# Optimization experiments

Hardware: AMD Instinct MI355X
Metric: run time of the kernel (lower is better)

The kernel has to match this reference:

```python
import jax, jax.numpy as jnp
import numpy as np
from jax import lax

MAX_SIGMA = 20.0
TRUNCATE = 4.0  # scipy.ndimage.gaussian_filter default
R = int(TRUNCATE * MAX_SIGMA + 0.5)  # fixed max radius = 80 -> 161 taps


def setup_inputs() -> dict:
    key = jax.random.key(0)
    k1, k2 = jax.random.split(key)
    x = jax.random.normal(k1, (512, 256, 256), dtype=jnp.float32)
    blur_sigmas = jnp.geomspace(0.5, MAX_SIGMA, 32).astype(jnp.float32)
    fwd_steps = jax.random.randint(k2, (512,), 0, 32)
    return {"x": x, "blur_sigmas": blur_sigmas, "fwd_steps": fwd_steps}


def _per_sample_kernels(sigmas):
    # scipy gaussian_filter: radius_i = int(truncate*sigma + 0.5), kernel
    # phi(o) = exp(-o^2 / (2 sigma^2)) normalized over |o| <= radius_i.
    off = jnp.arange(-R, R + 1, dtype=jnp.float32)          # [2R+1]
    w = jnp.exp(-0.5 * (off[None, :] / sigmas[:, None]) ** 2)  # [B, 2R+1]
    rad = jnp.floor(TRUNCATE * sigmas + 0.5)[:, None]        # per-sample radius
    w = w * (jnp.abs(off)[None, :] <= rad)
    return w / jnp.sum(w, axis=-1, keepdims=True)


def _blur(x, kernels):
    # x: [B, H, W]; kernels: [B, 2R+1]. Separable depthwise conv, batch as
    # channels with feature_group_count=B; symmetric pad == scipy 'reflect'.
    B = x.shape[0]
    dn = ("NCHW", "OIHW", "NCHW")
    xp = jnp.pad(x, ((0, 0), (R, R), (R, R)), mode="symmetric")[None]  # [1,B,H+2R,W+2R]
    kh = kernels[:, None, :, None]  # [B,1,2R+1,1]
    kw = kernels[:, None, None, :]  # [B,1,1,2R+1]
    y = lax.conv_general_dilated(xp, kh, (1, 1), "VALID",
                                 dimension_numbers=dn, feature_group_count=B)
    y = lax.conv_general_dilated(y, kw, (1, 1), "VALID",
                                 dimension_numbers=dn, feature_group_count=B)
    return y[0]  # [B, H, W]


def reference(x, blur_sigmas, fwd_steps):
    sigmas = blur_sigmas[fwd_steps]           # [B] per-sample sigma
    kernels = _per_sample_kernels(sigmas)     # [B, 2R+1]
    return _blur(x, kernels)
```

## Files before the change

kernel.cpp:

```cpp
#include <hip/hip_runtime.h>

#define WDIM  256
#define NSAMP 512
#define NSIG  32
#define RB    64
#define NBAND 2048
#define QOFF  16
#define WOFF  65536

typedef float    f32x4 __attribute__((ext_vector_type(4)));
typedef _Float16 f16x8 __attribute__((ext_vector_type(8)));

__device__ __forceinline__ int reflect(int q) {
    q = (q < 0) ? (-q - 1) : q;
    return (q >= WDIM) ? (2 * WDIM - 1 - q) : q;
}

__global__ __launch_bounds__(256) void build_w(const float* __restrict__ sigmas,
                                               _Float16* __restrict__ Wg) {
    __shared__ float wl[161];
    __shared__ float red;
    int s = blockIdx.x, t = threadIdx.x;
    float sigma = sigmas[s];
    float radf = floorf(4.0f * sigma + 0.5f);
    if (t < 161) {
        float off = (float)(t - 80);
        float w = 0.0f;
        if (fabsf(off) <= radf) { float z = off / sigma; w = expf(-0.5f * z * z); }
        wl[t] = w;
    }
    __syncthreads();
    if (t < 64) {
        float v = wl[t] + wl[t + 64] + (t < 33 ? wl[t + 128] : 0.0f);
        #pragma unroll
        for (int o = 32; o > 0; o >>= 1) v += __shfl_down(v, o);
        if (t == 0) red = 1.0f / v;
    }
    __syncthreads();
    float rs = red;
    int i = t;
    _Float16* wrow = Wg + ((size_t)s << 16) + (i << 8);
    for (int rq = blockIdx.y * 4; rq < blockIdx.y * 4 + 4; ++rq) {
        f16x8 v;
        #pragma unroll
        for (int j = 0; j < 8; ++j) {
            int r = rq * 8 + j;
            int d1 = r - i, d2 = -r - 1 - i, d3 = 511 - r - i;
            float w = 0.0f;
            if (d1 >= -80 && d1 <= 80) w += wl[d1 + 80];
            if (d2 >= -80)             w += wl[d2 + 80];
            if (d3 <= 80)              w += wl[d3 + 80];
            v[j] = (_Float16)(w * rs);
        }
        *(f16x8*)(wrow + rq * 8) = v;
    }
}

__global__ void build_queue(const float* __restrict__ sigmas,
                            const int* __restrict__ steps,
                            int* __restrict__ q) {
    __shared__ int hist[32];
    __shared__ int base[32];
    int t = threadIdx.x;
    if (t < 32) hist[t] = 0;
    __syncthreads();
    int nb2[2], rd2[2], st2[2];
    #pragma unroll
    for (int k = 0; k < 2; ++k) {
        int samp = t + 256 * k;
        int st = steps[samp];
        float sigma = sigmas[st];
        int rad = (int)floorf(4.0f * sigma + 0.5f);
        st2[k] = st; rd2[k] = rad;
        nb2[k] = (2 * rad + 15) >> 3;
        atomicAdd(&hist[nb2[k]], 1);
    }
    __syncthreads();
    if (t == 0) {
        int acc = 0;
        for (int bin = 31; bin >= 0; --bin) { base[bin] = acc; acc += hist[bin]; }
    }
    __syncthreads();
    #pragma unroll
    for (int k = 0; k < 2; ++k) {
        int samp = t + 256 * k;
        int r = atomicAdd(&base[nb2[k]], 1);
        int x = r & 7;
        int p = r >> 3;
        #pragma unroll
        for (int jb = 0; jb < 4; ++jb)
            q[QOFF + (((p << 2) + jb) << 3) + x] =
                samp | (jb << 9) | (st2[k] << 11) | (rd2[k] << 16);
    }
}

template <bool QUEUED>
__global__ __launch_bounds__(256, 2) void blur_mfma(const float* __restrict__ in,
                                                    float* __restrict__ out,
                                                    const float* __restrict__ sigmas,
                                                    const int* __restrict__ steps,
                                                    const int* __restrict__ q,
                                                    const _Float16* __restrict__ Wg) {
    __shared__ alignas(16) _Float16 YL[RB * WDIM];

    int b, r0, s, rad;
    if constexpr (QUEUED) {
        int d = q[QOFF + blockIdx.x];
        b   = d & 511;
        r0  = ((d >> 9) & 3) << 6;
        s   = (d >> 11) & 31;
        rad = (d >> 16) & 127;
    } else {
        int bid = blockIdx.x;
        int e = (bid & 7) * (NBAND / 8) + (bid >> 3);
        b = e >> 2; r0 = (e & 3) * RB;
        s = steps[b];
        rad = (int)floorf(4.0f * sigmas[s] + 0.5f);
    }
    const _Float16* Wm = Wg + ((size_t)s << 16);
    const float*    Xb = in + ((size_t)b << 16);

    int ln = threadIdx.x & 63, wv = threadIdx.x >> 6;
    int lm = ln & 15, lq = ln >> 4;

    f32x4 acc[4][4];
    #pragma unroll
    for (int mt = 0; mt < 4; ++mt)
        #pragma unroll
        for (int nt = 0; nt < 4; ++nt) acc[mt][nt] = (f32x4)0.0f;

    int kt0 = max(0, r0 - rad) >> 5;
    int kt1 = min(WDIM - 1, r0 + RB - 1 + rad) >> 5;

    float xvc[4][8], xvn[4][8];

    auto xload = [&](int kt, float (&dst)[4][8]) {
        const float* xp = Xb + (size_t)((kt << 5) + lq * 8) * WDIM + wv * 64 + lm;
        #pragma unroll
        for (int nt = 0; nt < 4; ++nt)
            #pragma unroll
            for (int jj = 0; jj < 8; ++jj)
                dst[nt][jj] = xp[(size_t)jj * WDIM + nt * 16];
    };
    auto vtile = [&](int kt, float (&xv)[4][8]) {
        f16x8 af[4];
        #pragma unroll
        for (int mt = 0; mt < 4; ++mt)
            af[mt] = *(const f16x8*)(Wm + (size_t)(r0 + mt * 16 + lm) * WDIM + (kt << 5) + lq * 8);
        #pragma unroll
        for (int nt = 0; nt < 4; ++nt) {
            f16x8 bf;
            #pragma unroll
            for (int jj = 0; jj < 8; ++jj) bf[jj] = (_Float16)xv[nt][jj];
            #pragma unroll
            for (int mt = 0; mt < 4; ++mt)
                acc[mt][nt] = __builtin_amdgcn_mfma_f32_16x16x32_f16(af[mt], bf, acc[mt][nt], 0, 0, 0);
        }
    };

    xload(kt0, xvc);
    for (int kt = kt0; kt <= kt1; ++kt) {
        if (kt < kt1) xload(kt + 1, xvn);
        vtile(kt, xvc);
        if (kt < kt1) {
            #pragma unroll
            for (int nt = 0; nt < 4; ++nt)
                #pragma unroll
                for (int jj = 0; jj < 8; ++jj) xvc[nt][jj] = xvn[nt][jj];
        }
    }

    #pragma unroll
    for (int mt = 0; mt < 4; ++mt)
        #pragma unroll
        for (int nt = 0; nt < 4; ++nt)
            #pragma unroll
            for (int g = 0; g < 4; ++g) {
                int i = mt * 16 + lq * 4 + g;
                int c = wv * 64 + nt * 16 + lm;
                YL[(i << 8) + (c ^ ((i & 7) << 3))] = (_Float16)acc[mt][nt][g];
            }

    int jlo = wv * 64;
    int hk0 = max(0, jlo - rad) >> 5;
    int hk1 = min(WDIM - 1, jlo + 63 + rad) >> 5;

    f16x8 bfc[4], bfn[4];
    auto wload = [&](int kt, f16x8 (&bf)[4]) {
        #pragma unroll
        for (int nt = 0; nt < 4; ++nt)
            bf[nt] = *(const f16x8*)(Wm + (size_t)(jlo + nt * 16 + lm) * WDIM + (kt << 5) + lq * 8);
    };
    wload(hk0, bfc);
    __syncthreads();

    f32x4 hac[4][4];
    #pragma unroll
    for (int mt = 0; mt < 4; ++mt)
        #pragma unroll
        for (int nt = 0; nt < 4; ++nt) hac[mt][nt] = (f32x4)0.0f;

    for (int kt = hk0; kt <= hk1; ++kt) {
        if (kt < hk1) wload(kt + 1, bfn);
        f16x8 af[4];
        #pragma unroll
        for (int mt = 0; mt < 4; ++mt) {
            int i = mt * 16 + lm;
            int c0 = (kt << 5) + lq * 8;
            af[mt] = *(const f16x8*)&YL[(i << 8) + (c0 ^ ((i & 7) << 3))];
        }
        #pragma unroll
        for (int mt = 0; mt < 4; ++mt)
            #pragma unroll
            for (int nt = 0; nt < 4; ++nt)
                hac[mt][nt] = __builtin_amdgcn_mfma_f32_16x16x32_f16(af[mt], bfc[nt], hac[mt][nt], 0, 0, 0);
        if (kt < hk1) {
            #pragma unroll
            for (int nt = 0; nt < 4; ++nt) bfc[nt] = bfn[nt];
        }
    }

    float* ob = out + ((size_t)b << 16);
    #pragma unroll
    for (int mt = 0; mt < 4; ++mt)
        #pragma unroll
        for (int nt = 0; nt < 4; ++nt)
            #pragma unroll
            for (int g = 0; g < 4; ++g)
                ob[(size_t)(r0 + mt * 16 + lq * 4 + g) * WDIM + jlo + nt * 16 + lm] = hac[mt][nt][g];
}

__device__ __forceinline__ int make_weights161(int b, const float* __restrict__ sigmas,
                                               const int* __restrict__ steps,
                                               float* wl, float* red) {
    int t = threadIdx.x;
    float sigma = sigmas[steps[b]];
    float radf = floorf(4.0f * sigma + 0.5f);
    if (t < 192) {
        float w = 0.0f;
        if (t < 161) {
            float off = (float)(t - 80);
            if (fabsf(off) <= radf) { float z = off / sigma; w = expf(-0.5f * z * z); }
        }
        wl[t] = w;
    }
    __syncthreads();
    if (t < 64) {
        float v = wl[t] + wl[t + 64] + wl[t + 128];
        #pragma unroll
        for (int o = 32; o > 0; o >>= 1) v += __shfl_down(v, o);
        if (t == 0) red[0] = 1.0f / v;
    }
    __syncthreads();
    float rs = red[0];
    if (t < 161) wl[t] *= rs;
    __syncthreads();
    return (int)radf;
}

__global__ __launch_bounds__(256) void vblur_nt(const float* __restrict__ in,
                                                float* __restrict__ out,
                                                const float* __restrict__ sigmas,
                                                const int* __restrict__ steps) {
    __shared__ float wl[192];
    __shared__ float red[1];
    int bid = blockIdx.x;
    int b = bid >> 4, i0 = (bid & 15) * 16;
    int rad = make_weights161(b, sigmas, steps, wl, red);
    int j = threadIdx.x;
    const float* inb = in + (size_t)b * WDIM * WDIM;
    float acc[16];
    #pragma unroll
    for (int ii = 0; ii < 16; ++ii) acc[ii] = 0.0f;
    for (int u = -rad; u <= rad; ++u) {
        float w = wl[80 + u];
        #pragma unroll
        for (int ii = 0; ii < 16; ++ii)
            acc[ii] = fmaf(w, inb[reflect(i0 + ii + u) * WDIM + j], acc[ii]);
    }
    #pragma unroll
    for (int ii = 0; ii < 16; ++ii)
        out[((size_t)b * WDIM + (i0 + ii)) * WDIM + j] = acc[ii];
}

__global__ __launch_bounds__(256) void hblur_inplace(float* __restrict__ buf,
                                                     const float* __restrict__ sigmas,
                                                     const int* __restrict__ steps) {
    __shared__ float wl[192];
    __shared__ float red[1];
    __shared__ float rp[WDIM + 160];
    int bid = blockIdx.x;
    int b = bid >> 8, i = bid & 255;
    float* row = buf + ((size_t)b * WDIM + i) * WDIM;
    int t = threadIdx.x;
    for (int s = t; s < WDIM + 160; s += 256) rp[s] = row[reflect(s - 80)];
    int rad = make_weights161(b, sigmas, steps, wl, red);
    float acc = 0.0f;
    for (int u = -rad; u <= rad; ++u) acc = fmaf(wl[80 + u], rp[80 + t + u], acc);
    row[t] = acc;
}

extern "C" void kernel_launch(void* const* d_in, const int* in_sizes, int n_in,
                              void* d_out, int out_size, void* d_ws, size_t ws_size,
                              hipStream_t stream) {
    const float* x     = (const float*)d_in[0];
    const float* sig   = (const float*)d_in[1];
    const int*   steps = (const int*)d_in[2];
    float* out = (float*)d_out;

    const size_t need = (size_t)WOFF + (size_t)NSIG * WDIM * WDIM * 2;
    if (ws_size >= need) {
        int* q = (int*)d_ws;
        _Float16* Wg = (_Float16*)((char*)d_ws + WOFF);
        build_w<<<dim3(NSIG, 8), 256, 0, stream>>>(sig, Wg);
        build_queue<<<1, 256, 0, stream>>>(sig, steps, q);
        blur_mfma<true><<<NBAND, 256, 0, stream>>>(x, out, sig, steps, q, Wg);
    } else {
        vblur_nt<<<NSAMP * 16, 256, 0, stream>>>(x, out, sig, steps);
        hblur_inplace<<<NSAMP * WDIM, 256, 0, stream>>>(out, sig, steps);
    }
}
```

Before: 84.90 us.

## Restructure MFMA blur to column-band tiles with LDS-staged inputs and fused setup

Each block now handles a 64-column band over all 256 rows. It runs the horizontal pass first, staging fp32 input tiles, converted to fp16, and the weight tiles through swizzled LDS with double-buffered register loads. It then runs the vertical pass from a transposed LDS buffer and skips K-tiles per 16-row subtile that fall outside the blur radius. The two setup kernels are merged into one launch, and occupancy is raised to 3 blocks per SU. The aims are coalesced global loads, fewer redundant weight loads and less wasted MFMA work, at the cost of more LDS, extra barriers per K-step and tighter register budgets.

```diff
diff --git a/kernel.cpp b/kernel.cpp
--- a/kernel.cpp
+++ b/kernel.cpp
@@ -3,231 +3,240 @@
 #define WDIM  256
 #define NSAMP 512
 #define NSIG  32
-#define RB    64
-#define NBAND 2048
+#define NBLK  2048
 #define QOFF  16
 #define WOFF  65536
 
 typedef float    f32x4 __attribute__((ext_vector_type(4)));
+typedef _Float16 f16x4 __attribute__((ext_vector_type(4)));
 typedef _Float16 f16x8 __attribute__((ext_vector_type(8)));
+typedef __fp16   fp16x2 __attribute__((ext_vector_type(2)));
 
 __device__ __forceinline__ int reflect(int q) {
     q = (q < 0) ? (-q - 1) : q;
     return (q >= WDIM) ? (2 * WDIM - 1 - q) : q;
 }
 
-__global__ __launch_bounds__(256) void build_w(const float* __restrict__ sigmas,
-                                               _Float16* __restrict__ Wg) {
-    __shared__ float wl[161];
-    __shared__ float red;
-    int s = blockIdx.x, t = threadIdx.x;
-    float sigma = sigmas[s];
-    float radf = floorf(4.0f * sigma + 0.5f);
-    if (t < 161) {
-        float off = (float)(t - 80);
-        float w = 0.0f;
-        if (fabsf(off) <= radf) { float z = off / sigma; w = expf(-0.5f * z * z); }
-        wl[t] = w;
-    }
-    __syncthreads();
-    if (t < 64) {
-        float v = wl[t] + wl[t + 64] + (t < 33 ? wl[t + 128] : 0.0f);
-        #pragma unroll
-        for (int o = 32; o > 0; o >>= 1) v += __shfl_down(v, o);
-        if (t == 0) red = 1.0f / v;
-    }
-    __syncthreads();
-    float rs = red;
-    int i = t;
-    _Float16* wrow = Wg + ((size_t)s << 16) + (i << 8);
-    for (int rq = blockIdx.y * 4; rq < blockIdx.y * 4 + 4; ++rq) {
-        f16x8 v;
-        #pragma unroll
-        for (int j = 0; j < 8; ++j) {
-            int r = rq * 8 + j;
-            int d1 = r - i, d2 = -r - 1 - i, d3 = 511 - r - i;
+__global__ __launch_bounds__(256) void build_all(const float* __restrict__ sigmas,
+                                                 const int* __restrict__ steps,
+                                                 _Float16* __restrict__ Wg,
+                                                 int* __restrict__ q) {
+    int t = threadIdx.x;
+    if (blockIdx.x < 256) {
+        __shared__ float wl[161];
+        __shared__ float red;
+        int s = blockIdx.x >> 3, og = blockIdx.x & 7;
+        float sigma = sigmas[s];
+        float radf = floorf(4.0f * sigma + 0.5f);
+        if (t < 161) {
+            float off = (float)(t - 80);
             float w = 0.0f;
-            if (d1 >= -80 && d1 <= 80) w += wl[d1 + 80];
-            if (d2 >= -80)             w += wl[d2 + 80];
-            if (d3 <= 80)              w += wl[d3 + 80];
-            v[j] = (_Float16)(w * rs);
-        }
-        *(f16x8*)(wrow + rq * 8) = v;
-    }
-}
-
-__global__ void build_queue(const float* __restrict__ sigmas,
-                            const int* __restrict__ steps,
-                            int* __restrict__ q) {
-    __shared__ int hist[32];
-    __shared__ int base[32];
-    int t = threadIdx.x;
-    if (t < 32) hist[t] = 0;
-    __syncthreads();
-    int nb2[2], rd2[2], st2[2];
-    #pragma unroll
-    for (int k = 0; k < 2; ++k) {
-        int samp = t + 256 * k;
-        int st = steps[samp];
-        float sigma = sigmas[st];
-        int rad = (int)floorf(4.0f * sigma + 0.5f);
-        st2[k] = st; rd2[k] = rad;
-        nb2[k] = (2 * rad + 15) >> 3;
-        atomicAdd(&hist[nb2[k]], 1);
-    }
-    __syncthreads();
-    if (t == 0) {
-        int acc = 0;
-        for (int bin = 31; bin >= 0; --bin) { base[bin] = acc; acc += hist[bin]; }
-    }
-    __syncthreads();
-    #pragma unroll
-    for (int k = 0; k < 2; ++k) {
-        int samp = t + 256 * k;
-        int r = atomicAdd(&base[nb2[k]], 1);
-        int x = r & 7;
-        int p = r >> 3;
-        #pragma unroll
-        for (int jb = 0; jb < 4; ++jb)
-            q[QOFF + (((p << 2) + jb) << 3) + x] =
-                samp | (jb << 9) | (st2[k] << 11) | (rd2[k] << 16);
+            if (fabsf(off) <= radf) { float z = off / sigma; w = expf(-0.5f * z * z); }
+            wl[t] = w;
+        }
+        __syncthreads();
+        if (t < 64) {
+            float v = wl[t] + wl[t + 64] + (t < 33 ? wl[t + 128] : 0.0f);
+            #pragma unroll
+            for (int o = 32; o > 0; o >>= 1) v += __shfl_down(v, o);
+            if (t == 0) red = 1.0f / v;
+        }
+        __syncthreads();
+        float rs = red;
+        int i = t;
+        _Float16* wrow = Wg + ((size_t)s << 16) + (i << 8);
+        for (int rq = og * 4; rq < og * 4 + 4; ++rq) {
+            f16x8 v;
+            #pragma unroll
+            for (int j = 0; j < 8; ++j) {
+                int r = rq * 8 + j;
+                int d1 = r - i, d2 = -r - 1 - i, d3 = 511 - r - i;
+                float w = 0.0f;
+                if (d1 >= -80 && d1 <= 80) w += wl[d1 + 80];
+                if (d2 >= -80)             w += wl[d2 + 80];
+                if (d3 <= 80)              w += wl[d3 + 80];
+                v[j] = (_Float16)(w * rs);
+            }
+            *(f16x8*)(wrow + rq * 8) = v;
+        }
+    } else {
+        __shared__ int hist[32];
+        __shared__ int base[32];
+        if (t < 32) hist[t] = 0;
+        __syncthreads();
+        int nb2[2], rd2[2], st2[2];
+        #pragma unroll
+        for (int k = 0; k < 2; ++k) {
+            int samp = t + 256 * k;
+            int st = steps[samp];
+            float sigma = sigmas[st];
+            int rad = (int)floorf(4.0f * sigma + 0.5f);
+            st2[k] = st; rd2[k] = rad;
+            nb2[k] = (2 * rad + 15) >> 3;
+            atomicAdd(&hist[nb2[k]], 1);
+        }
+        __syncthreads();
+        if (t == 0) {
+            int acc = 0;
+            for (int bin = 31; bin >= 0; --bin) { base[bin] = acc; acc += hist[bin]; }
+        }
+        __syncthreads();
+        #pragma unroll
+        for (int k = 0; k < 2; ++k) {
+            int samp = t + 256 * k;
+            int r = atomicAdd(&base[nb2[k]], 1);
+            int x = r & 7;
+            int p = r >> 3;
+            #pragma unroll
+            for (int jb = 0; jb < 4; ++jb)
+                q[QOFF + (((p << 2) + jb) << 3) + x] =
+                    samp | (jb << 9) | (st2[k] << 11) | (rd2[k] << 16);
+        }
     }
 }
 
 template <bool QUEUED>
-__global__ __launch_bounds__(256, 2) void blur_mfma(const float* __restrict__ in,
+__global__ __launch_bounds__(256, 3) void blur_mfma(const float* __restrict__ in,
                                                     float* __restrict__ out,
                                                     const float* __restrict__ sigmas,
                                                     const int* __restrict__ steps,
                                                     const int* __restrict__ q,
                                                     const _Float16* __restrict__ Wg) {
-    __shared__ alignas(16) _Float16 YL[RB * WDIM];
-
-    int b, r0, s, rad;
+    __shared__ alignas(16) _Float16 XL[256 * 32];
+    __shared__ alignas(16) _Float16 WH[64 * 32];
+    __shared__ alignas(16) _Float16 YT[64 * 256];
+
+    int b, j0, s, rad;
     if constexpr (QUEUED) {
         int d = q[QOFF + blockIdx.x];
         b   = d & 511;
-        r0  = ((d >> 9) & 3) << 6;
+        j0  = ((d >> 9) & 3) << 6;
         s   = (d >> 11) & 31;
         rad = (d >> 16) & 127;
     } else {
         int bid = blockIdx.x;
-        int e = (bid & 7) * (NBAND / 8) + (bid >> 3);
-        b = e >> 2; r0 = (e & 3) * RB;
+        int e = (bid & 7) * (NBLK / 8) + (bid >> 3);
+        b = e >> 2; j0 = (e & 3) << 6;
         s = steps[b];
         rad = (int)floorf(4.0f * sigmas[s] + 0.5f);
     }
     const _Float16* Wm = Wg + ((size_t)s << 16);
     const float*    Xb = in + ((size_t)b << 16);
 
-    int ln = threadIdx.x & 63, wv = threadIdx.x >> 6;
+    int tt = threadIdx.x;
+    int ln = tt & 63, wv = tt >> 6;
     int lm = ln & 15, lq = ln >> 4;
 
+    int sr = tt >> 3;
+    int sc = (tt & 7) * 4;
+    int sj = tt >> 2;
+    int sw8 = (tt & 3) * 8;
+
+    int kh0 = max(0, j0 - rad) >> 5;
+    int kh1 = min(WDIM - 1, j0 + 63 + rad) >> 5;
+
+    f32x4 xs[8];
+    f16x8 wst;
+    auto ldstage = [&](int kt) {
+        const float* xp = Xb + (size_t)sr * WDIM + (kt << 5) + sc;
+        #pragma unroll
+        for (int k = 0; k < 8; ++k)
+            xs[k] = *(const f32x4*)(xp + (size_t)(k * 32) * WDIM);
+        wst = *(const f16x8*)(Wm + (size_t)(j0 + sj) * WDIM + (kt << 5) + sw8);
+    };
+    auto wrstage = [&]() {
+        #pragma unroll
+        for (int k = 0; k < 8; ++k) {
+            int rr = sr + 32 * k;
+            union { f16x4 v; fp16x2 h[2]; } u;
+            u.h[0] = __builtin_amdgcn_cvt_pkrtz(xs[k][0], xs[k][1]);
+            u.h[1] = __builtin_amdgcn_cvt_pkrtz(xs[k][2], xs[k][3]);
+            *(f16x4*)&XL[rr * 32 + ((((sc >> 3) ^ (rr & 3)) << 3) + (sc & 7))] = u.v;
+        }
+        *(f16x8*)&WH[sj * 32 + (((tt & 3) ^ (sj & 3)) << 3)] = wst;
+    };
+
     f32x4 acc[4][4];
     #pragma unroll
     for (int mt = 0; mt < 4; ++mt)
         #pragma unroll
         for (int nt = 0; nt < 4; ++nt) acc[mt][nt] = (f32x4)0.0f;
 
-    int kt0 = max(0, r0 - rad) >> 5;
-    int kt1 = min(WDIM - 1, r0 + RB - 1 + rad) >> 5;
-
-    float xvc[4][8], xvn[4][8];
-
-    auto xload = [&](int kt, float (&dst)[4][8]) {
-        const float* xp = Xb + (size_t)((kt << 5) + lq * 8) * WDIM + wv * 64 + lm;
+    ldstage(kh0);
+    for (int kt = kh0; kt <= kh1; ++kt) {
+        wrstage();
+        __syncthreads();
+        if (kt < kh1) ldstage(kt + 1);
+        f16x8 bf[4];
+        #pragma unroll
+        for (int nt = 0; nt < 4; ++nt) {
+            int j = nt * 16 + lm;
+            bf[nt] = *(const f16x8*)&WH[j * 32 + ((lq ^ (j & 3)) << 3)];
+        }
+        #pragma unroll
+        for (int mt = 0; mt < 4; ++mt) {
+            int r = wv * 64 + mt * 16 + lm;
+            f16x8 af = *(const f16x8*)&XL[r * 32 + ((lq ^ (r & 3)) << 3)];
+            #pragma unroll
+            for (int nt = 0; nt < 4; ++nt)
+                acc[mt][nt] = __builtin_amdgcn_mfma_f32_16x16x32_f16(af, bf[nt], acc[mt][nt], 0, 0, 0);
+        }
+        __syncthreads();
+    }
+
+    #pragma unroll
+    for (int mt = 0; mt < 4; ++mt)
+        #pragma unroll
+        for (int nt = 0; nt < 4; ++nt) {
+            int r4 = wv * 64 + mt * 16 + lq * 4;
+            int j  = nt * 16 + lm;
+            union { f16x4 v; fp16x2 h[2]; } u;
+            u.h[0] = __builtin_amdgcn_cvt_pkrtz(acc[mt][nt][0], acc[mt][nt][1]);
+            u.h[1] = __builtin_amdgcn_cvt_pkrtz(acc[mt][nt][2], acc[mt][nt][3]);
+            *(f16x4*)&YT[j * 256 + ((((r4 >> 3) ^ (j & 7)) << 3) + (r4 & 7))] = u.v;
+        }
+    __syncthreads();
+
+    f32x4 hac[4][4];
+    #pragma unroll
+    for (int mt = 0; mt < 4; ++mt)
+        #pragma unroll
+        for (int nt = 0; nt < 4; ++nt) hac[mt][nt] = (f32x4)0.0f;
+
+    int ka[4], kb[4];
+    #pragma unroll
+    for (int mt = 0; mt < 4; ++mt) {
+        int i0m = wv * 64 + mt * 16;
+        ka[mt] = max(0, i0m - rad) >> 5;
+        kb[mt] = min(WDIM - 1, i0m + 15 + rad) >> 5;
+    }
+
+    for (int kt = ka[0]; kt <= kb[3]; ++kt) {
+        f16x8 bf[4];
+        #pragma unroll
+        for (int nt = 0; nt < 4; ++nt) {
+            int j = nt * 16 + lm;
+            bf[nt] = *(const f16x8*)&YT[j * 256 + ((((kt << 2) + lq) ^ (j & 7)) << 3)];
+        }
+        #pragma unroll
+        for (int mt = 0; mt < 4; ++mt) {
+            if (kt >= ka[mt] && kt <= kb[mt]) {
+                f16x8 af = *(const f16x8*)(Wm + (size_t)(wv * 64 + mt * 16 + lm) * WDIM + (kt << 5) + lq * 8);
+                #pragma unroll
+                for (int nt = 0; nt < 4; ++nt)
+                    hac[mt][nt] = __builtin_amdgcn_mfma_f32_16x16x32_f16(af, bf[nt], hac[mt][nt], 0, 0, 0);
+            }
+        }
+    }
+
+    float* ob = out + ((size_t)b << 16);
+    #pragma unroll
+    for (int mt = 0; mt < 4; ++mt)
         #pragma unroll
         for (int nt = 0; nt < 4; ++nt)
             #pragma unroll
-            for (int jj = 0; jj < 8; ++jj)
-                dst[nt][jj] = xp[(size_t)jj * WDIM + nt * 16];
-    };
-    auto vtile = [&](int kt, float (&xv)[4][8]) {
-        f16x8 af[4];
-        #pragma unroll
-        for (int mt = 0; mt < 4; ++mt)
-            af[mt] = *(const f16x8*)(Wm + (size_t)(r0 + mt * 16 + lm) * WDIM + (kt << 5) + lq * 8);
-        #pragma unroll
-        for (int nt = 0; nt < 4; ++nt) {
-            f16x8 bf;
-            #pragma unroll
-            for (int jj = 0; jj < 8; ++jj) bf[jj] = (_Float16)xv[nt][jj];
-            #pragma unroll
-            for (int mt = 0; mt < 4; ++mt)
-                acc[mt][nt] = __builtin_amdgcn_mfma_f32_16x16x32_f16(af[mt], bf, acc[mt][nt], 0, 0, 0);
-        }
-    };
-
-    xload(kt0, xvc);
-    for (int kt = kt0; kt <= kt1; ++kt) {
-        if (kt < kt1) xload(kt + 1, xvn);
-        vtile(kt, xvc);
-        if (kt < kt1) {
-            #pragma unroll
-            for (int nt = 0; nt < 4; ++nt)
-                #pragma unroll
-                for (int jj = 0; jj < 8; ++jj) xvc[nt][jj] = xvn[nt][jj];
-        }
-    }
-
-    #pragma unroll
-    for (int mt = 0; mt < 4; ++mt)
-        #pragma unroll
-        for (int nt = 0; nt < 4; ++nt)
-            #pragma unroll
-            for (int g = 0; g < 4; ++g) {
-                int i = mt * 16 + lq * 4 + g;
-                int c = wv * 64 + nt * 16 + lm;
-                YL[(i << 8) + (c ^ ((i & 7) << 3))] = (_Float16)acc[mt][nt][g];
-            }
-
-    int jlo = wv * 64;
-    int hk0 = max(0, jlo - rad) >> 5;
-    int hk1 = min(WDIM - 1, jlo + 63 + rad) >> 5;
-
-    f16x8 bfc[4], bfn[4];
-    auto wload = [&](int kt, f16x8 (&bf)[4]) {
-        #pragma unroll
-        for (int nt = 0; nt < 4; ++nt)
-            bf[nt] = *(const f16x8*)(Wm + (size_t)(jlo + nt * 16 + lm) * WDIM + (kt << 5) + lq * 8);
-    };
-    wload(hk0, bfc);
-    __syncthreads();
-
-    f32x4 hac[4][4];
-    #pragma unroll
-    for (int mt = 0; mt < 4; ++mt)
-        #pragma unroll
-        for (int nt = 0; nt < 4; ++nt) hac[mt][nt] = (f32x4)0.0f;
-
-    for (int kt = hk0; kt <= hk1; ++kt) {
-        if (kt < hk1) wload(kt + 1, bfn);
-        f16x8 af[4];
-        #pragma unroll
-        for (int mt = 0; mt < 4; ++mt) {
-            int i = mt * 16 + lm;
-            int c0 = (kt << 5) + lq * 8;
-            af[mt] = *(const f16x8*)&YL[(i << 8) + (c0 ^ ((i & 7) << 3))];
-        }
-        #pragma unroll
-        for (int mt = 0; mt < 4; ++mt)
-            #pragma unroll
-            for (int nt = 0; nt < 4; ++nt)
-                hac[mt][nt] = __builtin_amdgcn_mfma_f32_16x16x32_f16(af[mt], bfc[nt], hac[mt][nt], 0, 0, 0);
-        if (kt < hk1) {
-            #pragma unroll
-            for (int nt = 0; nt < 4; ++nt) bfc[nt] = bfn[nt];
-        }
-    }
-
-    float* ob = out + ((size_t)b << 16);
-    #pragma unroll
-    for (int mt = 0; mt < 4; ++mt)
-        #pragma unroll
-        for (int nt = 0; nt < 4; ++nt)
-            #pragma unroll
             for (int g = 0; g < 4; ++g)
-                ob[(size_t)(r0 + mt * 16 + lq * 4 + g) * WDIM + jlo + nt * 16 + lm] = hac[mt][nt][g];
+                ob[(size_t)(wv * 64 + mt * 16 + lq * 4 + g) * WDIM + j0 + nt * 16 + lm] = hac[mt][nt][g];
 }
 
 __device__ __forceinline__ int make_weights161(int b, const float* __restrict__ sigmas,
@@ -312,9 +321,8 @@
     if (ws_size >= need) {
         int* q = (int*)d_ws;
         _Float16* Wg = (_Float16*)((char*)d_ws + WOFF);
-        build_w<<<dim3(NSIG, 8), 256, 0, stream>>>(sig, Wg);
-        build_queue<<<1, 256, 0, stream>>>(sig, steps, q);
-        blur_mfma<true><<<NBAND, 256, 0, stream>>>(x, out, sig, steps, q, Wg);
+        build_all<<<257, 256, 0, stream>>>(sig, steps, Wg, q);
+        blur_mfma<true><<<NBLK, 256, 0, stream>>>(x, out, sig, steps, q, Wg);
     } else {
         vblur_nt<<<NSAMP * 16, 256, 0, stream>>>(x, out, sig, steps);
         hblur_inplace<<<NSAMP * WDIM, 256, 0, stream>>>(out, sig, steps);
```

Measured after the change: 73.45 us. 1.16x faster.
